# Optimization experiments

Measured on AMD Instinct MI355X. Metric: run time of the kernel, lower is better.

## Reference

```python
import jax, jax.numpy as jnp
import numpy as np
import math

B, T, D, M, V = 16, 256, 256, 32, 50257
EPS = 1e-6


def setup_inputs() -> dict:
    key = jax.random.key(0)
    ks = jax.random.split(key, 24)
    s = 0.02
    inp = {
        'hidden_state': jax.random.normal(ks[0], (B, 2, D), jnp.float32),
        'output_sequence': jax.random.randint(ks[1], (B, T), 0, V),
        # embedding table for output tokens
        'emb_out': jax.random.normal(ks[2], (V, D), jnp.float32) * s,
        # decoder_attention (Wq,Wk,Wv are torch Linear weights [out,in], plus biases)
        'Wq1': jax.random.normal(ks[3], (D, D), jnp.float32) * s,
        'bq1': jnp.zeros((D,), jnp.float32),
        'Wk1': jax.random.normal(ks[4], (D, D), jnp.float32) * s,
        'bk1': jnp.zeros((D,), jnp.float32),
        'Wv1': jax.random.normal(ks[5], (D, D), jnp.float32) * s,
        'bv1': jnp.zeros((D,), jnp.float32),
        # decoder_attention_2
        'Wq2': jax.random.normal(ks[6], (D, D), jnp.float32) * s,
        'bq2': jnp.zeros((D,), jnp.float32),
        'Wk2': jax.random.normal(ks[7], (D, D), jnp.float32) * s,
        'bk2': jnp.zeros((D,), jnp.float32),
        'Wv2': jax.random.normal(ks[8], (D, D), jnp.float32) * s,
        'bv2': jnp.zeros((D,), jnp.float32),
        # decoder_mover / decoder_mover_2 weights: nn.Linear(D, M).weight -> [M, D]
        'mover1': jax.random.normal(ks[9], (M, D), jnp.float32) * s,
        'mover2': jax.random.normal(ks[10], (M, D), jnp.float32) * s,
        # norm2
        'gamma': jnp.ones((D,), jnp.float32),
        'beta': jnp.zeros((D,), jnp.float32),
        # vocab logits linear [V, D] + bias
        'Wvoc': jax.random.normal(ks[11], (V, D), jnp.float32) * s,
        'bvoc': jnp.zeros((V,), jnp.float32),
    }
    return inp


def _attn(q, kv, Wq, bq, Wk, bk, Wv, bv):
    # q: [B,1,D], kv: [B,M+1,D]
    Q = q @ Wq.T + bq
    K = kv @ Wk.T + bk
    Vv = kv @ Wv.T + bv
    s = jnp.einsum('bqd,bkd->bqk', Q, K) / jnp.sqrt(jnp.asarray(Q.shape[-1], Q.dtype))
    a = jax.nn.softmax(s, axis=-1)
    return jnp.einsum('bqk,bkd->bqd', a, Vv)


def _layernorm(x, gamma, beta):
    mu = jnp.mean(x, axis=-1, keepdims=True)
    var = jnp.mean((x - mu) ** 2, axis=-1, keepdims=True)
    return (x - mu) * jax.lax.rsqrt(var + EPS) * gamma + beta


def reference(hidden_state, output_sequence, emb_out,
              Wq1, bq1, Wk1, bk1, Wv1, bv1,
              Wq2, bq2, Wk2, bk2, Wv2, bv2,
              mover1, mover2, gamma, beta, Wvoc, bvoc):
    d = emb_out.shape[1]
    # Embeddings: lookup scaled by sqrt(d) (standard simple-transformer embedding)
    x = emb_out[output_sequence] * jnp.sqrt(jnp.asarray(d, jnp.float32))  # [B,T,D]
    z0 = hidden_state[:, 0:1, :]
    z1 = hidden_state[:, 1:2, :]
    b = z0.shape[0]
    mv1 = jnp.broadcast_to(mover1[None], (b, mover1.shape[0], d))  # static per step
    mv2 = jnp.broadcast_to(mover2[None], (b, mover2.shape[0], d))

    def step(carry, xt):
        z0, z1 = carry
        z0 = z0 + xt[:, None, :]
        g = jnp.concatenate([z0, mv1], axis=1)          # [B,M+1,D]
        dg = _attn(g[:, :1], g, Wq1, bq1, Wk1, bk1, Wv1, bv1)
        g2 = jnp.concatenate([z1, mv2], axis=1)
        dg2 = _attn(g2[:, :1], g2, Wq2, bq2, Wk2, bk2, Wv2, bv2)
        z0 = _layernorm(z0 + dg + dg2, gamma, beta)
        return (z0, z0), None

    (z0, z1), _ = jax.lax.scan(step, (z0, z1), jnp.swapaxes(x, 0, 1))
    logits = z0 @ Wvoc.T + bvoc                         # [B,1,V]
    y = jax.nn.log_softmax(logits, axis=-1)
    return jnp.concatenate([z0, z1], axis=1), y
```

## Files before the change

### kernel.cpp

```cpp
#include <hip/hip_runtime.h>

typedef unsigned int u32;
typedef unsigned short u16;

#define DD 256
#define TT 256
#define MM 32
#define NBATCH 16
#define VV 50257

#define WS_FLAG   0
#define WS_KV     16
#define WS_A      32784
#define WS_W12S   163856
#define WS_CB     180240
#define WS_E12    180752
#define WS_CST    180816
#define WS_ZFIN   180832
#define WS_SSUM   184928
#define WS_WPK    184944
#define WS_US     332400
#define WS_SYNC   369264

#if defined(__has_builtin)
#if __has_builtin(__builtin_amdgcn_fdot2)
#define HAS_FDOT2 1
#endif
#endif

typedef _Float16 half2_t __attribute__((ext_vector_type(2)));

__device__ __forceinline__ float bf2f(u16 v){ return __uint_as_float(((u32)v) << 16); }
__device__ __forceinline__ float ldf(const void* p, size_t i, int bf){
  return bf ? bf2f(((const u16*)p)[i]) : ((const float*)p)[i];
}
__device__ __forceinline__ u32 packh2(float a, float b){
  union { half2_t h; u32 u; } x;
  x.h[0] = (_Float16)a; x.h[1] = (_Float16)b;
  return x.u;
}
__device__ __forceinline__ float fdot2(u32 a, u32 b, float c){
  union { u32 u; half2_t h; } ua, ub;
  ua.u = a; ub.u = b;
#ifdef HAS_FDOT2
  return __builtin_amdgcn_fdot2(ua.h, ub.h, c, false);
#else
  return c + (float)ua.h[0]*(float)ub.h[0] + (float)ua.h[1]*(float)ub.h[1];
#endif
}

__device__ __forceinline__ u32 ldu(const u32* p){
  return __hip_atomic_load(p, __ATOMIC_RELAXED, __HIP_MEMORY_SCOPE_SYSTEM);
}
__device__ __forceinline__ void stu(u32* p, u32 v){
  __hip_atomic_store(p, v, __ATOMIC_RELAXED, __HIP_MEMORY_SCOPE_SYSTEM);
}
template<bool FAST>
__device__ __forceinline__ u32 ldx(const u32* p){
  return __hip_atomic_load(p, __ATOMIC_RELAXED,
      FAST ? __HIP_MEMORY_SCOPE_AGENT : __HIP_MEMORY_SCOPE_SYSTEM);
}
template<bool FAST>
__device__ __forceinline__ void stx(u32* p, u32 v){
  __hip_atomic_store(p, v, __ATOMIC_RELAXED,
      FAST ? __HIP_MEMORY_SCOPE_AGENT : __HIP_MEMORY_SCOPE_SYSTEM);
}
template<bool FAST>
__device__ __forceinline__ void stx_tag(float* p, float v, u32 tag){
  stx<FAST>((u32*)p, (__float_as_uint(v) & ~1u) | tag);
}

__global__ __launch_bounds__(256) void k_init(const u32* gam, u32* flag,
                                              float* Ssum, u32* sync, u32* usg){
  const int gtid = blockIdx.x*256 + threadIdx.x;
  if (blockIdx.x == 0){
    if (threadIdx.x == 0) *flag = (gam[0] == 0x3F800000u) ? 0u : 1u;
    if (threadIdx.x < 16) Ssum[threadIdx.x] = 0.f;
    for (int i = threadIdx.x; i < 512; i += 256) stu(&sync[i], 0u);
  }
  for (int i = gtid; i < NBATCH*2304; i += 8*256) stu(&usg[i], 1u);
}

__global__ __launch_bounds__(256) void k_prep1(
  const void* Wk1, const void* bk1, const void* Wv1, const void* bv1,
  const void* Wk2, const void* bk2, const void* Wv2, const void* bv2,
  const void* m1, const void* m2, float* KV, const u32* flagp)
{
  const int bf = (int)*flagp;
  int mat = blockIdx.x >> 5, j = blockIdx.x & 31, d = threadIdx.x;
  const void *W, *bias, *mv;
  if (mat == 0){ W = Wk1; bias = bk1; mv = m1; }
  else if (mat == 1){ W = Wv1; bias = bv1; mv = m1; }
  else if (mat == 2){ W = Wk2; bias = bk2; mv = m2; }
  else { W = Wv2; bias = bv2; mv = m2; }
  float acc = ldf(bias, d, bf);
  for (int e = 0; e < DD; ++e) acc += ldf(W, d*DD + e, bf) * ldf(mv, j*DD + e, bf);
  KV[mat*8192 + j*DD + d] = acc;
}

__global__ __launch_bounds__(256) void k_prep2(
  const void* Wq1, const void* Wk1, const void* bq1, const void* bk1,
  const void* Wq2, const void* Wk2, const void* bq2, const void* bk2,
  const float* KV, float* A, float* W12s, float* cb, float* e12, float* cst,
  const u32* flagp)
{
  const int bf = (int)*flagp;
  int blk = blockIdx.x, tid = threadIdx.x;
  if (blk < 512){
    int mat = blk >> 8, i = blk & 255;
    const void* Wq = mat ? Wq2 : Wq1;
    const void* Wk = mat ? Wk2 : Wk1;
    float acc = 0.f;
    for (int e = 0; e < DD; ++e) acc += ldf(Wq, e*DD + i, bf) * ldf(Wk, e*DD + tid, bf);
    A[mat*65536 + i*DD + tid] = acc;
  } else if (blk < 576){
    int idx = blk - 512, mat = idx >> 5, j = idx & 31;
    const void* Wq = mat ? Wq2 : Wq1;
    const float* K = KV + mat*16384;
    float acc = 0.f;
    for (int e = 0; e < DD; ++e) acc += ldf(Wq, e*DD + tid, bf) * K[j*DD + e];
    W12s[mat*8192 + j*DD + tid] = acc;
  } else if (blk < 578){
    int mat = blk - 576;
    const void* Wq = mat ? Wq2 : Wq1;
    const void* Wk = mat ? Wk2 : Wk1;
    const void* bq = mat ? bq2 : bq1;
    const void* bk = mat ? bk2 : bk1;
    float acc = 0.f;
    for (int e = 0; e < DD; ++e)
      acc += ldf(Wk, e*DD + tid, bf) * ldf(bq, e, bf) + ldf(Wq, e*DD + tid, bf) * ldf(bk, e, bf);
    cb[mat*DD + tid] = acc;
  } else {
    if (tid < 32){
      float acc = 0.f;
      for (int d = 0; d < DD; ++d) acc += ldf(bq1, d, bf) * KV[tid*DD + d];
      e12[tid] = acc;
    } else if (tid < 64){
      int j = tid - 32; float acc = 0.f;
      for (int d = 0; d < DD; ++d) acc += ldf(bq2, d, bf) * KV[16384 + j*DD + d];
      e12[32 + j] = acc;
    } else if (tid == 64){
      float acc = 0.f;
      for (int d = 0; d < DD; ++d) acc += ldf(bq1, d, bf) * ldf(bk1, d, bf);
      cst[0] = acc;
    } else if (tid == 65){
      float acc = 0.f;
      for (int d = 0; d < DD; ++d) acc += ldf(bq2, d, bf) * ldf(bk2, d, bf);
      cst[1] = acc;
    }
  }
}

__global__ __launch_bounds__(256) void k_pack(
  const float* __restrict__ A, const float* __restrict__ W12s,
  const float* __restrict__ cb, const void* __restrict__ Wv1,
  const void* __restrict__ Wv2, u32* __restrict__ Wpk, const u32* flagp)
{
  const int bf = (int)*flagp;
  int idx = blockIdx.x*256 + threadIdx.x;
  float v0 = 0.f, v1 = 0.f;
  if (idx < 131072){
    int p = idx >> 15;
    int r2 = idx & 32767;
    int e2g = r2 >> 10;
    int t = (r2 >> 2) & 255;
    int q = r2 & 3;
    int c = e2g*8 + q*2;
    if (p == 0){ v0 = A[t*DD + c]; v1 = A[t*DD + c + 1]; }
    else if (p == 1){ v0 = ldf(Wv1, t*DD + c, bf); v1 = ldf(Wv1, t*DD + c + 1, bf); }
    else if (p == 2){ v0 = A[65536 + t*DD + c]; v1 = A[65536 + t*DD + c + 1]; }
    else { v0 = ldf(Wv2, t*DD + c, bf); v1 = ldf(Wv2, t*DD + c + 1, bf); }
  } else {
    int rem = idx - 131072;
    int t = rem >> 7;
    int e2g = (rem >> 2) & 31;
    int q = rem & 3;
    int c = e2g*8 + q*2;
    if (t < 32){ v0 = W12s[t*DD + c]; v1 = W12s[t*DD + c + 1]; }
    else if (t < 64){ v0 = W12s[8192 + (t-32)*DD + c]; v1 = W12s[8192 + (t-32)*DD + c + 1]; }
    else if (t == 64){ v0 = cb[c]; v1 = cb[c + 1]; }
    else if (t == 65){ v0 = cb[DD + c]; v1 = cb[DD + c + 1]; }
  }
  Wpk[idx] = packh2(v0, v1);
}

template<bool FAST>
__device__ __forceinline__ void seq_loop(
    int tid, int g, int b, int lane, int wv, int bf,
    float* us0, float* us1,
    const uint4* wpMain, const uint4* wpP4, bool p4z1, int p4row, int xi,
    const void* emb, const int* toks, float c1, float c2,
    float* z0s, float* z1s, u32* zp0, u32* zp1,
    const u32* V1h, const u32* V2h,
    float* a1s, float* a2s, float* red,
    const float* gs, const float* bs, const float* bv1s, const float* bv2s,
    const float* e1s, const float* e2s,
    float* zfin, float* out0)
{
  for (int t = 0; t < TT; ++t){
    float* usw = (t & 1) ? us1 : us0;
    const u32 tg = (u32)((t >> 1) & 1);
    float xnext = 0.f;
    if (t + 1 < TT) xnext = ldf(emb, (size_t)toks[t+1]*DD + tid, bf) * 16.0f;

    if (tid < 128) zp0[tid] = packh2(z0s[2*tid], z0s[2*tid+1]);
    else { int i = tid - 128; zp1[i] = packh2(z1s[2*i], z1s[2*i+1]); }
    __syncthreads();

    {
      const uint4* zp4 = (const uint4*)((g < 2) ? zp0 : zp1);
      float a0 = 0.f, a1 = 0.f, a2 = 0.f, a3 = 0.f;
      #pragma unroll 8
      for (int k = 0; k < 32; ++k){
        uint4 w = wpMain[k*256];
        uint4 z = zp4[k];
        a0 = fdot2(w.x, z.x, a0);
        a1 = fdot2(w.y, z.y, a1);
        a2 = fdot2(w.z, z.z, a2);
        a3 = fdot2(w.w, z.w, a3);
      }
      stx_tag<FAST>(&usw[g*256 + tid], (a0 + a1) + (a2 + a3), tg);
    }
    {
      const uint4* zq = (const uint4*)(p4z1 ? zp1 : zp0);
      float a0 = 0.f, a1 = 0.f, a2 = 0.f, a3 = 0.f;
      #pragma unroll
      for (int j = 0; j < 4; ++j){
        uint4 w = wpP4[j*8];
        uint4 z = zq[(tid & 7) + 8*j];
        a0 = fdot2(w.x, z.x, a0);
        a1 = fdot2(w.y, z.y, a1);
        a2 = fdot2(w.z, z.z, a2);
        a3 = fdot2(w.w, z.w, a3);
      }
      float s = (a0 + a1) + (a2 + a3);
      s += __shfl_down(s, 4, 64);
      s += __shfl_down(s, 2, 64);
      s += __shfl_down(s, 1, 64);
      if ((tid & 7) == 0) stx_tag<FAST>(&usw[1024 + p4row], s, tg);
    }

    u32 b0, b1, b2, b3, bx;
    {
      const u32* up = (const u32*)usw;
      for (;;){
        b0 = ldx<FAST>(up + tid);
        b1 = ldx<FAST>(up + 256 + tid);
        b2 = ldx<FAST>(up + 512 + tid);
        b3 = ldx<FAST>(up + 768 + tid);
        bx = ldx<FAST>(up + xi);
        if ((((b0 ^ tg) | (b1 ^ tg) | (b2 ^ tg) | (b3 ^ tg) | (bx ^ tg)) & 1u) == 0u)
          break;
      }
    }
    float u0  = __uint_as_float(b0);
    float uv1 = __uint_as_float(b1);
    float u2  = __uint_as_float(b2);
    float uv2 = __uint_as_float(b3);
    float xf  = __uint_as_float(bx);

    float p1 = z0s[tid] * u0;
    float p2 = z1s[tid] * u2;
    #pragma unroll
    for (int off = 32; off; off >>= 1){
      p1 += __shfl_down(p1, off, 64);
      p2 += __shfl_down(p2, off, 64);
    }
    if (lane == 0){ red[wv] = p1; red[4 + wv] = p2; }
    __syncthreads();
    if (tid == 0) a1s[0] = (red[0]+red[1]+red[2]+red[3] + xf + c1) * 0.0625f;
    if (tid == 1) a2s[0] = (red[4]+red[5]+red[6]+red[7] + xf + c2) * 0.0625f;
    if (tid >= 64 && tid < 96)  a1s[tid - 63] = (xf + e1s[tid-64]) * 0.0625f;
    if (tid >= 96 && tid < 128) a2s[tid - 95] = (xf + e2s[tid-96]) * 0.0625f;
    __syncthreads();

    if (tid < 128){
      float* sm = (tid < 64) ? a1s : a2s;
      float v = (lane < 33) ? sm[lane] : -1e30f;
      float mx = v;
      #pragma unroll
      for (int off = 32; off; off >>= 1) mx = fmaxf(mx, __shfl_xor(mx, off, 64));
      float e = (lane < 33) ? expf(v - mx) : 0.f;
      float s = e;
      #pragma unroll
      for (int off = 32; off; off >>= 1) s += __shfl_xor(s, off, 64);
      if (lane < 33) sm[lane] = e / s;
    }
    __syncthreads();

    float hv1 = __uint_as_float(b1) + bv1s[tid];
    float hv2 = uv2 + bv2s[tid];
    (void)uv1;
    float dg = a1s[0] * hv1;
    float dh = a2s[0] * hv2;
    int half_idx = tid >> 1;
    #pragma unroll
    for (int j = 1; j <= 32; ++j){
      union { u32 u; half2_t h; } pv1, pv2;
      pv1.u = V1h[((j-1) << 7) + half_idx];
      pv2.u = V2h[((j-1) << 7) + half_idx];
      float e1v = (tid & 1) ? (float)pv1.h[1] : (float)pv1.h[0];
      float e2v = (tid & 1) ? (float)pv2.h[1] : (float)pv2.h[0];
      dg += a1s[j] * e1v;
      dh += a2s[j] * e2v;
    }
    float y = z0s[tid] + dg + dh;
    float sy = y, syy = y * y;
    #pragma unroll
    for (int off = 32; off; off >>= 1){
      sy += __shfl_down(sy, off, 64);
      syy += __shfl_down(syy, off, 64);
    }
    if (lane == 0){ red[8 + wv] = sy; red[12 + wv] = syy; }
    __syncthreads();
    float Sy = red[8] + red[9] + red[10] + red[11];
    float Syy = red[12] + red[13] + red[14] + red[15];
    float mu = Sy * (1.f/DD);
    float var = Syy * (1.f/DD) - mu*mu;
    float zi = (y - mu) * rsqrtf(var + 1e-6f) * gs[tid] + bs[tid];
    if (t == TT - 1){
      if (g == 0){
        zfin[b*DD + tid] = zi;
        out0[b*2*DD + tid] = zi;
        out0[b*2*DD + DD + tid] = zi;
      }
    } else {
      z1s[tid] = zi;
      z0s[tid] = zi + xnext;
    }
    __syncthreads();
  }

  const u32 P = 0x7fffffffu;
  stx<FAST>((u32*)&us0[g*256 + tid], P);
  stx<FAST>((u32*)&us1[g*256 + tid], P);
  if ((tid & 7) == 0){
    stx<FAST>((u32*)&us0[1024 + p4row], P);
    stx<FAST>((u32*)&us1[1024 + p4row], P);
  }
}

__global__ __launch_bounds__(256) void k_seq(
    const void* __restrict__ hid, const int* __restrict__ seq,
    const void* __restrict__ emb,
    const u32* __restrict__ Wpk, const float* __restrict__ V1g,
    const float* __restrict__ V2g, const float* __restrict__ e1g,
    const float* __restrict__ e2g_, const float* __restrict__ cst,
    const void* __restrict__ bv1, const void* __restrict__ bv2,
    const void* __restrict__ gam, const void* __restrict__ bet,
    float* __restrict__ zfin, float* __restrict__ out0,
    const u32* __restrict__ flagp, float* __restrict__ usg,
    u32* __restrict__ syncg)
{
  __shared__ float z0s[DD], z1s[DD];
  __shared__ __align__(16) u32 zp0[128], zp1[128];
  __shared__ u32 V1h[MM*DD/2], V2h[MM*DD/2];
  __shared__ float a1s[33], a2s[33];
  __shared__ float red[16];
  __shared__ float gs[DD], bs[DD], bv1s[DD], bv2s[DD];
  __shared__ float e1s[MM], e2s[MM];
  __shared__ int toks[TT];
  __shared__ u32 fastsh;

  const int tid = threadIdx.x;
  const int wg = blockIdx.x;
  const int b = wg & 15;
  const int g = wg >> 4;
  const int lane = tid & 63;
  const int wv = tid >> 6;
  const int bf = (int)*flagp;

  float* us0 = usg + b*2304;
  float* us1 = us0 + 1152;
  u32* det = syncg + b*8;

  u32 myxcd = 0;
  asm volatile("s_getreg_b32 %0, hwreg(HW_REG_XCC_ID)" : "=s"(myxcd));
  if (tid == 0){
    stu(&det[g], myxcd + 1u);
    u32 v0, v1, v2, v3;
    do {
      v0 = ldu(&det[0]); v1 = ldu(&det[1]);
      v2 = ldu(&det[2]); v3 = ldu(&det[3]);
    } while (!(v0 && v1 && v2 && v3));
    fastsh = (v0 == v1 && v1 == v2 && v2 == v3) ? 1u : 0u;
  }

  for (int r = tid; r < MM*DD/2; r += 256){
    V1h[r] = packh2(V1g[2*r], V1g[2*r + 1]);
    V2h[r] = packh2(V2g[2*r], V2g[2*r + 1]);
  }
  for (int r = tid; r < TT; r += 256) toks[r] = seq[b*TT + r];
  gs[tid] = ldf(gam, tid, bf); bs[tid] = ldf(bet, tid, bf);
  bv1s[tid] = ldf(bv1, tid, bf); bv2s[tid] = ldf(bv2, tid, bf);
  if (tid < MM){ e1s[tid] = e1g[tid]; e2s[tid] = e2g_[tid]; }
  const float c1 = cst[0], c2 = cst[1];
  __syncthreads();
  z1s[tid] = ldf(hid, b*2*DD + DD + tid, bf);
  z0s[tid] = ldf(hid, b*2*DD + tid, bf) + ldf(emb, (size_t)toks[0]*DD + tid, bf) * 16.0f;
  const bool fast = (fastsh != 0);
  __syncthreads();

  const uint4* Wp = (const uint4*)Wpk;
  const uint4* wpMain = Wp + g*8192 + tid;
  const int p4row = g*32 + (tid >> 3);
  const uint4* wpP4 = Wp + 32768 + p4row*32 + (tid & 7);
  const bool p4z1 = (p4row >= 32 && p4row < 64) || (p4row == 65);

  int xi;
  if (tid < 2) xi = 1088 + tid;
  else if (tid >= 64 && tid < 128) xi = 1024 + (tid - 64);
  else xi = tid;

  if (fast)
    seq_loop<true >(tid, g, b, lane, wv, bf, us0, us1, wpMain, wpP4, p4z1, p4row, xi,
                    emb, toks, c1, c2, z0s, z1s, zp0, zp1, V1h, V2h, a1s, a2s, red,
                    gs, bs, bv1s, bv2s, e1s, e2s, zfin, out0);
  else
    seq_loop<false>(tid, g, b, lane, wv, bf, us0, us1, wpMain, wpP4, p4z1, p4row, xi,
                    emb, toks, c1, c2, z0s, z1s, zp0, zp1, V1h, V2h, a1s, a2s, red,
                    gs, bs, bv1s, bv2s, e1s, e2s, zfin, out0);
}

__global__ __launch_bounds__(256) void k_logits(
    const float* __restrict__ zfin, const void* __restrict__ Wvoc,
    const void* __restrict__ bvoc, float* __restrict__ Ssum,
    float* __restrict__ out1, const u32* __restrict__ flagp)
{
  __shared__ float zfs[NBATCH][DD];
  const int tid = threadIdx.x;
  const int bf = (int)*flagp;
  for (int r = tid; r < NBATCH*DD; r += 256) zfs[r >> 8][r & 255] = zfin[r];
  __syncthreads();

  const int v = blockIdx.x*256 + tid;
  float acc[NBATCH];
  const bool ok = (v < VV);
  float bias = ok ? ldf(bvoc, v, bf) : 0.f;
  #pragma unroll
  for (int b = 0; b < NBATCH; ++b) acc[b] = bias;

  if (ok){
    if (bf){
      const uint4* wr = ((const uint4*)Wvoc) + (size_t)v*32;
      for (int gg = 0; gg < 32; ++gg){
        uint4 u = wr[gg];
        float w0 = __uint_as_float(u.x << 16), w1 = __uint_as_float(u.x & 0xffff0000u);
        float w2 = __uint_as_float(u.y << 16), w3 = __uint_as_float(u.y & 0xffff0000u);
        float w4 = __uint_as_float(u.z << 16), w5 = __uint_as_float(u.z & 0xffff0000u);
        float w6 = __uint_as_float(u.w << 16), w7 = __uint_as_float(u.w & 0xffff0000u);
        const int c = gg*8;
        #pragma unroll
        for (int b = 0; b < NBATCH; ++b){
          const float* zc = &zfs[b][c];
          acc[b] += w0*zc[0] + w1*zc[1] + w2*zc[2] + w3*zc[3]
                  + w4*zc[4] + w5*zc[5] + w6*zc[6] + w7*zc[7];
        }
      }
    } else {
      const float4* wr = ((const float4*)Wvoc) + (size_t)v*64;
      for (int gg = 0; gg < 64; ++gg){
        float4 u = wr[gg];
        const int c = gg*4;
        #pragma unroll
        for (int b = 0; b < NBATCH; ++b){
          const float* zc = &zfs[b][c];
          acc[b] += u.x*zc[0] + u.y*zc[1] + u.z*zc[2] + u.w*zc[3];
        }
      }
    }
    #pragma unroll
    for (int b = 0; b < NBATCH; ++b) out1[(size_t)b*VV + v] = acc[b];
  }

  #pragma unroll
  for (int b = 0; b < NBATCH; ++b){
    float p = ok ? expf(acc[b]) : 0.f;
    #pragma unroll
    for (int off = 32; off; off >>= 1) p += __shfl_down(p, off, 64);
    if ((tid & 63) == 0) atomicAdd(&Ssum[b], p);
  }
}

__global__ __launch_bounds__(256) void k_final(
    const float* __restrict__ Ssum, float* __restrict__ out1)
{
  const int v = blockIdx.x*256 + threadIdx.x;
  const int b = blockIdx.y;
  if (v < VV){
    float ls = logf(Ssum[b]);
    size_t i = (size_t)b*VV + v;
    out1[i] = out1[i] - ls;
  }
}

extern "C" void kernel_launch(void* const* d_in, const int* in_sizes, int n_in,
                              void* d_out, int out_size, void* d_ws, size_t ws_size,
                              hipStream_t stream)
{
  (void)in_sizes; (void)n_in; (void)out_size; (void)ws_size;
  const void* hid  = d_in[0];
  const int*  seq  = (const int*)d_in[1];
  const void* emb  = d_in[2];
  const void* Wq1  = d_in[3];
  const void* bq1  = d_in[4];
  const void* Wk1  = d_in[5];
  const void* bk1  = d_in[6];
  const void* Wv1  = d_in[7];
  const void* bv1  = d_in[8];
  const void* Wq2  = d_in[9];
  const void* bq2  = d_in[10];
  const void* Wk2  = d_in[11];
  const void* bk2  = d_in[12];
  const void* Wv2  = d_in[13];
  const void* bv2  = d_in[14];
  const void* m1   = d_in[15];
  const void* m2   = d_in[16];
  const void* gam  = d_in[17];
  const void* bet  = d_in[18];
  const void* Wvoc = d_in[19];
  const void* bvoc = d_in[20];

  float* wsf    = (float*)d_ws;
  u32*   flag   = (u32*)(wsf + WS_FLAG);
  float* KV     = wsf + WS_KV;
  float* A      = wsf + WS_A;
  float* W12s   = wsf + WS_W12S;
  float* cb     = wsf + WS_CB;
  float* e12    = wsf + WS_E12;
  float* cst    = wsf + WS_CST;
  float* zfin   = wsf + WS_ZFIN;
  float* Ssum   = wsf + WS_SSUM;
  u32*   Wpk    = (u32*)(wsf + WS_WPK);
  float* usg    = wsf + WS_US;
  u32*   syncg  = (u32*)(wsf + WS_SYNC);

  float* out0 = (float*)d_out;
  float* out1 = out0 + NBATCH*2*DD;

  k_init<<<8, 256, 0, stream>>>((const u32*)gam, flag, Ssum, syncg, (u32*)usg);
  k_prep1<<<128, 256, 0, stream>>>(Wk1,bk1,Wv1,bv1,Wk2,bk2,Wv2,bv2,m1,m2,KV,flag);
  k_prep2<<<579, 256, 0, stream>>>(Wq1,Wk1,bq1,bk1,Wq2,Wk2,bq2,bk2,KV,A,W12s,cb,e12,cst,flag);
  k_pack<<<576, 256, 0, stream>>>(A,W12s,cb,Wv1,Wv2,Wpk,flag);
  k_seq<<<NBATCH*4, 256, 0, stream>>>(hid, seq, emb, Wpk, KV+8192, KV+24576,
                                      e12, e12+32, cst, bv1, bv2, gam, bet, zfin, out0,
                                      flag, usg, syncg);
  k_logits<<<197, 256, 0, stream>>>(zfin, Wvoc, bvoc, Ssum, out1, flag);
  k_final<<<dim3(197, NBATCH), 256, 0, stream>>>(Ssum, out1);
}
```

Measured before the change: 1.758 ms.

## Split sequential recurrence across eight workgroups per batch with LDS-resident weight slices

```diff
diff --git a/kernel.cpp b/kernel.cpp
--- a/kernel.cpp
+++ b/kernel.cpp
@@ -186,17 +186,20 @@
 
 template<bool FAST>
 __device__ __forceinline__ void seq_loop(
-    int tid, int g, int b, int lane, int wv, int bf,
+    int tid, int b, int lane, int wv, int bf,
+    int p, int h, int rl, int c, int l, int p4row, bool p4act, bool p4z1, int xi,
     float* us0, float* us1,
-    const uint4* wpMain, const uint4* wpP4, bool p4z1, int p4row, int xi,
+    const uint4* Wsl, const uint4* P4sl,
     const void* emb, const int* toks, float c1, float c2,
     float* z0s, float* z1s, u32* zp0, u32* zp1,
-    const u32* V1h, const u32* V2h,
+    const u32* V1q, const u32* V2q,
     float* a1s, float* a2s, float* red,
     const float* gs, const float* bs, const float* bv1s, const float* bv2s,
     const float* e1s, const float* e2s,
-    float* zfin, float* out0)
-{
+    float* zfin, float* out0, int g)
+{
+  const int hi = tid >> 1;
+  const int sel = tid & 1;
   for (int t = 0; t < TT; ++t){
     float* usw = (t & 1) ? us1 : us0;
     const u32 tg = (u32)((t >> 1) & 1);
@@ -208,36 +211,42 @@
     __syncthreads();
 
     {
-      const uint4* zp4 = (const uint4*)((g < 2) ? zp0 : zp1);
+      const uint4* zz = ((const uint4*)((p < 2) ? zp0 : zp1)) + c*16;
+      const uint4* wr = Wsl + c*2048 + rl;
       float a0 = 0.f, a1 = 0.f, a2 = 0.f, a3 = 0.f;
       #pragma unroll 8
-      for (int k = 0; k < 32; ++k){
-        uint4 w = wpMain[k*256];
-        uint4 z = zp4[k];
-        a0 = fdot2(w.x, z.x, a0);
-        a1 = fdot2(w.y, z.y, a1);
-        a2 = fdot2(w.z, z.z, a2);
-        a3 = fdot2(w.w, z.w, a3);
-      }
-      stx_tag<FAST>(&usw[g*256 + tid], (a0 + a1) + (a2 + a3), tg);
-    }
-    {
-      const uint4* zq = (const uint4*)(p4z1 ? zp1 : zp0);
-      float a0 = 0.f, a1 = 0.f, a2 = 0.f, a3 = 0.f;
-      #pragma unroll
-      for (int j = 0; j < 4; ++j){
-        uint4 w = wpP4[j*8];
-        uint4 z = zq[(tid & 7) + 8*j];
+      for (int kk = 0; kk < 16; ++kk){
+        uint4 w = wr[kk*128];
+        uint4 z = zz[kk];
         a0 = fdot2(w.x, z.x, a0);
         a1 = fdot2(w.y, z.y, a1);
         a2 = fdot2(w.z, z.z, a2);
         a3 = fdot2(w.w, z.w, a3);
       }
       float s = (a0 + a1) + (a2 + a3);
-      s += __shfl_down(s, 4, 64);
-      s += __shfl_down(s, 2, 64);
-      s += __shfl_down(s, 1, 64);
-      if ((tid & 7) == 0) stx_tag<FAST>(&usw[1024 + p4row], s, tg);
+      s += __shfl_down(s, 1, 2);
+      if (c == 0) stx_tag<FAST>(&usw[p*256 + h*128 + rl], s, tg);
+    }
+    if (p4act){
+      const uint4* zq4 = (const uint4*)(p4z1 ? zp1 : zp0);
+      uint4 w0 = P4sl[(tid >> 4 << 5) + l*2];
+      uint4 w1 = P4sl[(tid >> 4 << 5) + l*2 + 1];
+      uint4 za = zq4[l*2];
+      uint4 zb = zq4[l*2 + 1];
+      float a0 = fdot2(w0.x, za.x, 0.f);
+      float a1 = fdot2(w0.y, za.y, 0.f);
+      a0 = fdot2(w0.z, za.z, a0);
+      a1 = fdot2(w0.w, za.w, a1);
+      a0 = fdot2(w1.x, zb.x, a0);
+      a1 = fdot2(w1.y, zb.y, a1);
+      a0 = fdot2(w1.z, zb.z, a0);
+      a1 = fdot2(w1.w, zb.w, a1);
+      float s = a0 + a1;
+      s += __shfl_down(s, 8, 16);
+      s += __shfl_down(s, 4, 16);
+      s += __shfl_down(s, 2, 16);
+      s += __shfl_down(s, 1, 16);
+      if (l == 0) stx_tag<FAST>(&usw[1024 + p4row], s, tg);
     }
 
     u32 b0, b1, b2, b3, bx;
@@ -288,21 +297,25 @@
     }
     __syncthreads();
 
-    float hv1 = __uint_as_float(b1) + bv1s[tid];
+    float hv1 = uv1 + bv1s[tid];
     float hv2 = uv2 + bv2s[tid];
-    (void)uv1;
     float dg = a1s[0] * hv1;
     float dh = a2s[0] * hv2;
-    int half_idx = tid >> 1;
+    const uint4* v1p = (const uint4*)(V1q + hi*36);
+    const uint4* v2p = (const uint4*)(V2q + hi*36);
     #pragma unroll
-    for (int j = 1; j <= 32; ++j){
-      union { u32 u; half2_t h; } pv1, pv2;
-      pv1.u = V1h[((j-1) << 7) + half_idx];
-      pv2.u = V2h[((j-1) << 7) + half_idx];
-      float e1v = (tid & 1) ? (float)pv1.h[1] : (float)pv1.h[0];
-      float e2v = (tid & 1) ? (float)pv2.h[1] : (float)pv2.h[0];
-      dg += a1s[j] * e1v;
-      dh += a2s[j] * e2v;
+    for (int jj = 0; jj < 8; ++jj){
+      uint4 w1 = v1p[jj];
+      uint4 w2 = v2p[jj];
+      union { u32 u; half2_t hh; } cv;
+      cv.u = w1.x; dg += a1s[4*jj+1] * (sel ? (float)cv.hh[1] : (float)cv.hh[0]);
+      cv.u = w1.y; dg += a1s[4*jj+2] * (sel ? (float)cv.hh[1] : (float)cv.hh[0]);
+      cv.u = w1.z; dg += a1s[4*jj+3] * (sel ? (float)cv.hh[1] : (float)cv.hh[0]);
+      cv.u = w1.w; dg += a1s[4*jj+4] * (sel ? (float)cv.hh[1] : (float)cv.hh[0]);
+      cv.u = w2.x; dh += a2s[4*jj+1] * (sel ? (float)cv.hh[1] : (float)cv.hh[0]);
+      cv.u = w2.y; dh += a2s[4*jj+2] * (sel ? (float)cv.hh[1] : (float)cv.hh[0]);
+      cv.u = w2.z; dh += a2s[4*jj+3] * (sel ? (float)cv.hh[1] : (float)cv.hh[0]);
+      cv.u = w2.w; dh += a2s[4*jj+4] * (sel ? (float)cv.hh[1] : (float)cv.hh[0]);
     }
     float y = z0s[tid] + dg + dh;
     float sy = y, syy = y * y;
@@ -332,9 +345,11 @@
   }
 
   const u32 P = 0x7fffffffu;
-  stx<FAST>((u32*)&us0[g*256 + tid], P);
-  stx<FAST>((u32*)&us1[g*256 + tid], P);
-  if ((tid & 7) == 0){
+  if (c == 0){
+    stx<FAST>((u32*)&us0[p*256 + h*128 + rl], P);
+    stx<FAST>((u32*)&us1[p*256 + h*128 + rl], P);
+  }
+  if (p4act && l == 0){
     stx<FAST>((u32*)&us0[1024 + p4row], P);
     stx<FAST>((u32*)&us1[1024 + p4row], P);
   }
@@ -352,9 +367,11 @@
     const u32* __restrict__ flagp, float* __restrict__ usg,
     u32* __restrict__ syncg)
 {
+  __shared__ uint4 Wsl[4096];
+  __shared__ uint4 P4sl[512];
+  __shared__ u32 V1q[128*36], V2q[128*36];
   __shared__ float z0s[DD], z1s[DD];
   __shared__ __align__(16) u32 zp0[128], zp1[128];
-  __shared__ u32 V1h[MM*DD/2], V2h[MM*DD/2];
   __shared__ float a1s[33], a2s[33];
   __shared__ float red[16];
   __shared__ float gs[DD], bs[DD], bv1s[DD], bv2s[DD];
@@ -366,29 +383,46 @@
   const int wg = blockIdx.x;
   const int b = wg & 15;
   const int g = wg >> 4;
+  const int p = g >> 1;
+  const int h = g & 1;
+  const int rl = tid >> 1;
+  const int c = tid & 1;
   const int lane = tid & 63;
   const int wv = tid >> 6;
   const int bf = (int)*flagp;
 
   float* us0 = usg + b*2304;
   float* us1 = us0 + 1152;
-  u32* det = syncg + b*8;
+  u32* det = syncg + b*32;
 
   u32 myxcd = 0;
   asm volatile("s_getreg_b32 %0, hwreg(HW_REG_XCC_ID)" : "=s"(myxcd));
   if (tid == 0){
     stu(&det[g], myxcd + 1u);
-    u32 v0, v1, v2, v3;
-    do {
-      v0 = ldu(&det[0]); v1 = ldu(&det[1]);
-      v2 = ldu(&det[2]); v3 = ldu(&det[3]);
-    } while (!(v0 && v1 && v2 && v3));
-    fastsh = (v0 == v1 && v1 == v2 && v2 == v3) ? 1u : 0u;
-  }
-
-  for (int r = tid; r < MM*DD/2; r += 256){
-    V1h[r] = packh2(V1g[2*r], V1g[2*r + 1]);
-    V2h[r] = packh2(V2g[2*r], V2g[2*r + 1]);
+    for (;;){
+      u32 v0 = ldu(&det[0]), v1 = ldu(&det[1]), v2 = ldu(&det[2]), v3 = ldu(&det[3]);
+      u32 v4 = ldu(&det[4]), v5 = ldu(&det[5]), v6 = ldu(&det[6]), v7 = ldu(&det[7]);
+      if (v0 && v1 && v2 && v3 && v4 && v5 && v6 && v7){
+        fastsh = (v0==v1 && v1==v2 && v2==v3 && v3==v4 && v4==v5 && v5==v6 && v6==v7)
+                 ? 1u : 0u;
+        break;
+      }
+    }
+  }
+
+  const uint4* Wp = (const uint4*)Wpk;
+  for (int i = tid; i < 4096; i += 256){
+    int kk = i >> 7, rr = i & 127;
+    Wsl[kk*128 + rr] = Wp[p*8192 + kk*256 + h*128 + rr];
+  }
+  for (int i = tid; i < 512; i += 256){
+    int rr = i >> 5, ee = i & 31;
+    P4sl[rr*32 + ee] = Wp[32768 + (g*16 + rr)*32 + ee];
+  }
+  for (int i = tid; i < 4096; i += 256){
+    int hi2 = i >> 5, j = i & 31;
+    V1q[hi2*36 + j] = packh2(V1g[j*DD + 2*hi2], V1g[j*DD + 2*hi2 + 1]);
+    V2q[hi2*36 + j] = packh2(V2g[j*DD + 2*hi2], V2g[j*DD + 2*hi2 + 1]);
   }
   for (int r = tid; r < TT; r += 256) toks[r] = seq[b*TT + r];
   gs[tid] = ldf(gam, tid, bf); bs[tid] = ldf(bet, tid, bf);
@@ -401,10 +435,9 @@
   const bool fast = (fastsh != 0);
   __syncthreads();
 
-  const uint4* Wp = (const uint4*)Wpk;
-  const uint4* wpMain = Wp + g*8192 + tid;
-  const int p4row = g*32 + (tid >> 3);
-  const uint4* wpP4 = Wp + 32768 + p4row*32 + (tid & 7);
+  const int p4row = g*16 + (tid >> 4);
+  const int l = tid & 15;
+  const bool p4act = (p4row < 66);
   const bool p4z1 = (p4row >= 32 && p4row < 64) || (p4row == 65);
 
   int xi;
@@ -413,13 +446,15 @@
   else xi = tid;
 
   if (fast)
-    seq_loop<true >(tid, g, b, lane, wv, bf, us0, us1, wpMain, wpP4, p4z1, p4row, xi,
-                    emb, toks, c1, c2, z0s, z1s, zp0, zp1, V1h, V2h, a1s, a2s, red,
-                    gs, bs, bv1s, bv2s, e1s, e2s, zfin, out0);
+    seq_loop<true >(tid, b, lane, wv, bf, p, h, rl, c, l, p4row, p4act, p4z1, xi,
+                    us0, us1, Wsl, P4sl, emb, toks, c1, c2, z0s, z1s, zp0, zp1,
+                    V1q, V2q, a1s, a2s, red, gs, bs, bv1s, bv2s, e1s, e2s,
+                    zfin, out0, g);
   else
-    seq_loop<false>(tid, g, b, lane, wv, bf, us0, us1, wpMain, wpP4, p4z1, p4row, xi,
-                    emb, toks, c1, c2, z0s, z1s, zp0, zp1, V1h, V2h, a1s, a2s, red,
-                    gs, bs, bv1s, bv2s, e1s, e2s, zfin, out0);
+    seq_loop<false>(tid, b, lane, wv, bf, p, h, rl, c, l, p4row, p4act, p4z1, xi,
+                    us0, us1, Wsl, P4sl, emb, toks, c1, c2, z0s, z1s, zp0, zp1,
+                    V1q, V2q, a1s, a2s, red, gs, bs, bv1s, bv2s, e1s, e2s,
+                    zfin, out0, g);
 }
 
 __global__ __launch_bounds__(256) void k_logits(
@@ -449,10 +484,10 @@
         float w2 = __uint_as_float(u.y << 16), w3 = __uint_as_float(u.y & 0xffff0000u);
         float w4 = __uint_as_float(u.z << 16), w5 = __uint_as_float(u.z & 0xffff0000u);
         float w6 = __uint_as_float(u.w << 16), w7 = __uint_as_float(u.w & 0xffff0000u);
-        const int c = gg*8;
+        const int cc = gg*8;
         #pragma unroll
         for (int b = 0; b < NBATCH; ++b){
-          const float* zc = &zfs[b][c];
+          const float* zc = &zfs[b][cc];
           acc[b] += w0*zc[0] + w1*zc[1] + w2*zc[2] + w3*zc[3]
                   + w4*zc[4] + w5*zc[5] + w6*zc[6] + w7*zc[7];
         }
@@ -461,10 +496,10 @@
       const float4* wr = ((const float4*)Wvoc) + (size_t)v*64;
       for (int gg = 0; gg < 64; ++gg){
         float4 u = wr[gg];
-        const int c = gg*4;
+        const int cc = gg*4;
         #pragma unroll
         for (int b = 0; b < NBATCH; ++b){
-          const float* zc = &zfs[b][c];
+          const float* zc = &zfs[b][cc];
           acc[b] += u.x*zc[0] + u.y*zc[1] + u.z*zc[2] + u.w*zc[3];
         }
       }
@@ -475,10 +510,10 @@
 
   #pragma unroll
   for (int b = 0; b < NBATCH; ++b){
-    float p = ok ? expf(acc[b]) : 0.f;
+    float pp = ok ? expf(acc[b]) : 0.f;
     #pragma unroll
-    for (int off = 32; off; off >>= 1) p += __shfl_down(p, off, 64);
-    if ((tid & 63) == 0) atomicAdd(&Ssum[b], p);
+    for (int off = 32; off; off >>= 1) pp += __shfl_down(pp, off, 64);
+    if ((tid & 63) == 0) atomicAdd(&Ssum[b], pp);
   }
 }
 
@@ -542,7 +577,7 @@
   k_prep1<<<128, 256, 0, stream>>>(Wk1,bk1,Wv1,bv1,Wk2,bk2,Wv2,bv2,m1,m2,KV,flag);
   k_prep2<<<579, 256, 0, stream>>>(Wq1,Wk1,bq1,bk1,Wq2,Wk2,bq2,bk2,KV,A,W12s,cb,e12,cst,flag);
   k_pack<<<576, 256, 0, stream>>>(A,W12s,cb,Wv1,Wv2,Wpk,flag);
-  k_seq<<<NBATCH*4, 256, 0, stream>>>(hid, seq, emb, Wpk, KV+8192, KV+24576,
+  k_seq<<<NBATCH*8, 256, 0, stream>>>(hid, seq, emb, Wpk, KV+8192, KV+24576,
                                       e12, e12+32, cst, bv1, bv2, gam, bet, zfin, out0,
                                       flag, usg, syncg);
   k_logits<<<197, 256, 0, stream>>>(zfin, Wvoc, bvoc, Ssum, out1, flag);
```

Result: faster. 1.666 ms (-5.2%).
